# Kernel tuning notes

Measured on AMD Instinct MI355X. Metric: run time of the kernel, lower is better.

The kernel has to match this reference:

```python
import jax, jax.numpy as jnp
import numpy as np

THRESHOLD = 0.1  # init kwarg threshold
N_HITS_PER_EVENT = 200000
N_EVENTS = 64


def setup_inputs() -> dict:
    key = jax.random.key(0)
    n = N_HITS_PER_EVENT * N_EVENTS
    score = jax.random.uniform(key, (n, 1), dtype=jnp.float32)  # noise score in (0,1)
    row_splits = (jnp.arange(N_EVENTS + 1, dtype=jnp.int32) * N_HITS_PER_EVENT)
    return {"score": score, "row_splits": row_splits}


def reference(score, row_splits):
    """Faithful, fully vectorized version of select_threshold_with_backgather.

    Per segment: keep all vertices with score > threshold PLUS all vertices tied
    with the segment minimum score; non-kept vertices backgather to the FIRST
    kept minimum-score vertex of their segment (new/compacted indexing).
    Returns (sel [M,1], newrs [n_seg+1], backgather [N,1]) in the layer's
    call-output order (sel, newrs, allbackgather).
    """
    s = score[:, 0]
    n = s.shape[0]
    n_seg = row_splits.shape[0] - 1

    # segment id of every vertex from the row splits
    segids = jnp.searchsorted(row_splits, jnp.arange(n, dtype=row_splits.dtype), side='right') - 1
    segids = segids.astype(jnp.int32)

    # per-segment minimum score; ties with the min are all kept (== original isminscore)
    segmin = jax.ops.segment_min(s, segids, num_segments=n_seg)
    ismin = s == segmin[segids]
    keep = (s > THRESHOLD) | ismin

    # global compacted position of each kept vertex (n_previous_rs + local keeprange)
    kept_pos = jnp.cumsum(keep.astype(jnp.int32)) - 1

    # representative = first kept min-score vertex per segment (original minidx + n_previous_rs)
    big = jnp.int32(n)
    rep_pos = jax.ops.segment_min(jnp.where(keep & ismin, kept_pos, big), segids, num_segments=n_seg)

    backgather = jnp.where(keep, kept_pos, rep_pos[segids])

    # selection indices (data-dependent size; computed on concrete values, not under jit)
    sel = jnp.nonzero(keep)[0].astype(jnp.int32)

    counts = jax.ops.segment_sum(keep.astype(jnp.int32), segids, num_segments=n_seg)
    newrs = jnp.concatenate([jnp.zeros((1,), jnp.int32), jnp.cumsum(counts).astype(jnp.int32)])

    return sel[:, None], newrs, backgather[:, None].astype(jnp.int32)
```

## Files before the change

kernel.cpp:

```cpp
#include <hip/hip_runtime.h>
#include <stdint.h>

#define BLOCK 256
#define ITEMS 8
#define TILE (BLOCK * ITEMS)
#define WPB (TILE / 64)
#define MAXSEG 64
#define THRESH 0.1f

typedef unsigned long long u64;

__device__ __forceinline__ int find_seg(const int* rs, int n_seg, int i) {
    int lo = 0, hi = n_seg;
    while (hi - lo > 1) {
        int mid = (lo + hi) >> 1;
        if (rs[mid] <= i) lo = mid; else hi = mid;
    }
    return lo;
}

__global__ __launch_bounds__(BLOCK) void k_pass1(const float* __restrict__ score,
        const int* __restrict__ row_splits, int n_seg, int n, int nwords,
        u64* __restrict__ partial_val, int* __restrict__ partial_seg,
        u64* __restrict__ bitmask, int* __restrict__ block_counts) {
    __shared__ int rs[MAXSEG + 1];
    __shared__ u64 wval[8];
    __shared__ int wseg[8];
    __shared__ int wsum[4];
    for (int j = threadIdx.x; j <= n_seg; j += BLOCK) rs[j] = row_splits[j];
    __syncthreads();
    int lane = threadIdx.x & 63, wv = threadIdx.x >> 6;
    int wbase = blockIdx.x * TILE + wv * 512;
    u64 m0 = ~0ull, m1 = ~0ull, myword = 0;
    int sf = -1, sl = -1, cnt = 0;
    if (wbase < n) {
        int wend = min(n, wbase + 512) - 1;
        sf = find_seg(rs, n_seg, wbase);
        sl = find_seg(rs, n_seg, wend);
        int bval = (sl != sf) ? rs[sf + 1] : 0x7FFFFFFF;
        #pragma unroll
        for (int it = 0; it < 8; it++) {
            int i = wbase + it * 64 + lane;
            bool keep = false;
            if (i < n) {
                float v = score[i];
                u64 p = ((u64)__float_as_uint(v) << 32) | (unsigned int)i;
                if (i < bval) m0 = min(m0, p); else m1 = min(m1, p);
                keep = v > THRESH;
            }
            u64 bal = __ballot(keep);
            if (lane == it) myword = bal;
            cnt += __popcll(bal);
        }
        for (int o = 32; o > 0; o >>= 1) {
            m0 = min(m0, (u64)__shfl_down((unsigned long long)m0, o, 64));
            m1 = min(m1, (u64)__shfl_down((unsigned long long)m1, o, 64));
        }
        if (lane < 8) {
            int w = (wbase >> 6) + lane;
            if (w < nwords) bitmask[w] = myword;
        }
    }
    if (lane == 0) {
        wval[2 * wv] = m0;     wseg[2 * wv] = sf;
        wval[2 * wv + 1] = m1; wseg[2 * wv + 1] = (sl != sf) ? sl : -1;
        wsum[wv] = cnt;
    }
    __syncthreads();
    if (threadIdx.x == 0) {
        int base = blockIdx.x * TILE;
        int endi = min(n, base + TILE) - 1;
        int s0 = find_seg(rs, n_seg, base);
        int s1 = find_seg(rs, n_seg, endi);
        u64 o0 = ~0ull, o1 = ~0ull;
        for (int k = 0; k < 8; k++) {
            if (wseg[k] == s0) o0 = min(o0, wval[k]);
            else if (wseg[k] == s1) o1 = min(o1, wval[k]);
        }
        partial_val[2 * blockIdx.x] = o0;
        partial_seg[2 * blockIdx.x] = s0;
        partial_val[2 * blockIdx.x + 1] = o1;
        partial_seg[2 * blockIdx.x + 1] = (s1 != s0) ? s1 : -1;
        block_counts[blockIdx.x] = wsum[0] + wsum[1] + wsum[2] + wsum[3];
    }
}

__global__ __launch_bounds__(BLOCK) void k_segfix(const float* __restrict__ score,
        const int* __restrict__ row_splits, int n_seg, int n,
        const u64* __restrict__ partial_val, const int* __restrict__ partial_seg,
        u64* __restrict__ seg_packed, u64* __restrict__ bitmask,
        int* __restrict__ block_counts) {
    __shared__ u64 wred[4];
    __shared__ int nmatch;
    __shared__ int mlist[64];
    int s = blockIdx.x;
    int lo = row_splits[s], hi = row_splits[s + 1];
    int lane = threadIdx.x & 63, wv = threadIdx.x >> 6;
    if (threadIdx.x == 0) nmatch = 0;
    u64 m = ~0ull;
    int e0 = 0, e1 = -1;
    if (hi > lo) {
        e0 = 2 * (lo / TILE);
        e1 = 2 * ((hi - 1) / TILE) + 1;
        for (int e = e0 + threadIdx.x; e <= e1; e += BLOCK)
            if (partial_seg[e] == s) m = min(m, partial_val[e]);
    }
    for (int o = 32; o > 0; o >>= 1)
        m = min(m, (u64)__shfl_down((unsigned long long)m, o, 64));
    if (lane == 0) wred[wv] = m;
    __syncthreads();
    if (threadIdx.x == 0) {
        u64 r = min(min(wred[0], wred[1]), min(wred[2], wred[3]));
        wred[0] = r;
        seg_packed[s] = r;
    }
    __syncthreads();
    u64 sp = wred[0];
    if (sp == ~0ull) return;
    unsigned int smb = (unsigned int)(sp >> 32);
    if (__uint_as_float(smb) > THRESH) return;
    for (int e = e0 + threadIdx.x; e <= e1; e += BLOCK) {
        if (partial_seg[e] == s && (unsigned int)(partial_val[e] >> 32) == smb) {
            int k = atomicAdd(&nmatch, 1);
            if (k < 64) mlist[k] = e >> 1;
        }
    }
    __syncthreads();
    int nm = min(nmatch, 64);
    for (int k = 0; k < nm; k++) {
        int b = mlist[k];
        int rlo = max(b * TILE, lo);
        int rhi = min(min((b + 1) * TILE, n), hi);
        int c = 0;
        for (int i = rlo + threadIdx.x; i < rhi; i += BLOCK) {
            if (__float_as_uint(score[i]) == smb) {
                atomicOr(&bitmask[i >> 6], 1ull << (i & 63));
                c++;
            }
        }
        for (int o = 32; o > 0; o >>= 1) c += __shfl_down(c, o, 64);
        if (lane == 0 && c) atomicAdd(&block_counts[b], c);
    }
}

__global__ __launch_bounds__(BLOCK) void k_scan(const int* __restrict__ counts,
                                                int* __restrict__ offsets, int nb) {
    __shared__ int wtot[BLOCK / 64];
    int per = (nb + BLOCK - 1) / BLOCK;
    int s = per * threadIdx.x, e = min(nb, s + per);
    int sum = 0;
    for (int i = s; i < e; i++) sum += counts[i];
    int lane = threadIdx.x & 63, wv = threadIdx.x >> 6;
    int incl = sum;
    for (int o = 1; o < 64; o <<= 1) {
        int t = __shfl_up(incl, o, 64);
        if (lane >= o) incl += t;
    }
    if (lane == 63) wtot[wv] = incl;
    __syncthreads();
    int excl = incl - sum;
    for (int k = 0; k < wv; k++) excl += wtot[k];
    for (int i = s; i < e; i++) { offsets[i] = excl; excl += counts[i]; }
}

__global__ __launch_bounds__(BLOCK) void k_query(const int* __restrict__ row_splits,
        int n_seg, int n, int M,
        const u64* __restrict__ seg_packed, const u64* __restrict__ bitmask,
        const int* __restrict__ block_offsets,
        int* __restrict__ rep_pos, int* __restrict__ newrs_out) {
    int lane = threadIdx.x & 63, wv = threadIdx.x >> 6;
    int q = blockIdx.x * (BLOCK / 64) + wv;
    int nq = 2 * n_seg + 1;
    if (q >= nq) return;
    unsigned int uidx;
    if (q <= n_seg) uidx = (unsigned int)row_splits[q];
    else uidx = (unsigned int)(seg_packed[q - (n_seg + 1)] & 0xFFFFFFFFu);
    int result;
    if (uidx >= (unsigned int)n) {
        result = M;
    } else {
        int idx = (int)uidx;
        int b = idx / TILE;
        int wq = idx >> 6;
        int cnt = 0;
        for (int w = b * WPB + lane; w < wq; w += 64) cnt += __popcll(bitmask[w]);
        if (lane == 0 && (idx & 63))
            cnt += __popcll(bitmask[wq] & ((1ull << (idx & 63)) - 1));
        for (int o = 32; o > 0; o >>= 1) cnt += __shfl_down(cnt, o, 64);
        result = block_offsets[b] + cnt;
    }
    if (lane == 0) {
        if (q <= n_seg) newrs_out[q] = result;
        else rep_pos[q - (n_seg + 1)] = result;
    }
}

__global__ __launch_bounds__(BLOCK) void k_output(const int* __restrict__ row_splits,
        int n_seg, int n,
        const int* __restrict__ rep_pos, const u64* __restrict__ bitmask,
        const int* __restrict__ block_offsets,
        int* __restrict__ sel_out, int* __restrict__ back_out) {
    __shared__ int rs[MAXSEG + 1];
    __shared__ int srep[MAXSEG];
    __shared__ u64 swords[WPB];
    __shared__ int wpre[WPB];
    for (int j = threadIdx.x; j <= n_seg; j += BLOCK) rs[j] = row_splits[j];
    for (int j = threadIdx.x; j < n_seg; j += BLOCK) srep[j] = rep_pos[j];
    int base = blockIdx.x * TILE;
    int nw = min(WPB, (n - base + 63) >> 6);
    for (int j = threadIdx.x; j < nw; j += BLOCK) swords[j] = bitmask[(base >> 6) + j];
    __syncthreads();
    if (threadIdx.x == 0) {
        int acc = 0;
        for (int k = 0; k < nw; k++) { wpre[k] = acc; acc += __popcll(swords[k]); }
    }
    __syncthreads();
    int bo = block_offsets[blockIdx.x];
    int lane = threadIdx.x & 63, wv = threadIdx.x >> 6;
    #pragma unroll
    for (int it = 0; it < 8; it++) {
        int widx = wv * 8 + it;
        int i = base + widx * 64 + lane;
        if (i < n) {
            u64 word = swords[widx];
            bool keep = (word >> lane) & 1;
            int val;
            if (keep) {
                int pos = bo + wpre[widx] + __popcll(word & ((1ull << lane) - 1));
                val = pos;
                sel_out[pos] = i;
            } else {
                int seg = find_seg(rs, n_seg, i);
                val = srep[seg];
            }
            back_out[i] = val;
        }
    }
}

extern "C" void kernel_launch(void* const* d_in, const int* in_sizes, int n_in,
                              void* d_out, int out_size, void* d_ws, size_t ws_size,
                              hipStream_t stream) {
    const float* score = (const float*)d_in[0];
    const int* row_splits = (const int*)d_in[1];
    int n = in_sizes[0];
    int n_seg = in_sizes[1] - 1;
    int M = out_size - (n_seg + 1) - n;
    int nb = (n + TILE - 1) / TILE;
    int nwords = (n + 63) / 64;

    u64* seg_packed   = (u64*)d_ws;
    u64* partial_val  = seg_packed + MAXSEG;
    int* partial_seg  = (int*)(partial_val + 2 * nb);
    int* rep_pos      = partial_seg + 2 * nb;
    int* block_counts = rep_pos + 64;
    int* block_offsets= block_counts + nb;
    uintptr_t bm_addr = (uintptr_t)(block_offsets + nb);
    bm_addr = (bm_addr + 7) & ~(uintptr_t)7;
    u64* bitmask      = (u64*)bm_addr;

    int* out = (int*)d_out;
    int* sel_out   = out;
    int* newrs_out = out + M;
    int* back_out  = out + M + (n_seg + 1);

    hipLaunchKernelGGL(k_pass1, dim3(nb), dim3(BLOCK), 0, stream,
                       score, row_splits, n_seg, n, nwords,
                       partial_val, partial_seg, bitmask, block_counts);
    hipLaunchKernelGGL(k_segfix, dim3(n_seg), dim3(BLOCK), 0, stream,
                       score, row_splits, n_seg, n,
                       partial_val, partial_seg, seg_packed, bitmask, block_counts);
    hipLaunchKernelGGL(k_scan, dim3(1), dim3(BLOCK), 0, stream,
                       block_counts, block_offsets, nb);
    int nq = 2 * n_seg + 1;
    int qblocks = (nq + (BLOCK / 64) - 1) / (BLOCK / 64);
    hipLaunchKernelGGL(k_query, dim3(qblocks), dim3(BLOCK), 0, stream,
                       row_splits, n_seg, n, M, seg_packed, bitmask,
                       block_offsets, rep_pos, newrs_out);
    hipLaunchKernelGGL(k_output, dim3(nb), dim3(BLOCK), 0, stream,
                       row_splits, n_seg, n, rep_pos, bitmask,
                       block_offsets, sel_out, back_out);
}
```

Baseline: 186.9 us.

## Fuse scan with query kernel and stage output writes through shared memory

```diff
diff --git a/kernel.cpp b/kernel.cpp
--- a/kernel.cpp
+++ b/kernel.cpp
@@ -143,53 +143,48 @@
     }
 }
 
-__global__ __launch_bounds__(BLOCK) void k_scan(const int* __restrict__ counts,
-                                                int* __restrict__ offsets, int nb) {
+__global__ __launch_bounds__(BLOCK) void k_scanq(const int* __restrict__ counts,
+        int* __restrict__ offsets, int nb,
+        const int* __restrict__ row_splits, int n_seg, int n, int M,
+        const u64* __restrict__ seg_packed, const u64* __restrict__ bitmask,
+        int* __restrict__ rep_pos, int* __restrict__ newrs_out) {
     __shared__ int wtot[BLOCK / 64];
-    int per = (nb + BLOCK - 1) / BLOCK;
-    int s = per * threadIdx.x, e = min(nb, s + per);
-    int sum = 0;
-    for (int i = s; i < e; i++) sum += counts[i];
     int lane = threadIdx.x & 63, wv = threadIdx.x >> 6;
-    int incl = sum;
-    for (int o = 1; o < 64; o <<= 1) {
-        int t = __shfl_up(incl, o, 64);
-        if (lane >= o) incl += t;
-    }
-    if (lane == 63) wtot[wv] = incl;
-    __syncthreads();
-    int excl = incl - sum;
-    for (int k = 0; k < wv; k++) excl += wtot[k];
-    for (int i = s; i < e; i++) { offsets[i] = excl; excl += counts[i]; }
-}
-
-__global__ __launch_bounds__(BLOCK) void k_query(const int* __restrict__ row_splits,
-        int n_seg, int n, int M,
-        const u64* __restrict__ seg_packed, const u64* __restrict__ bitmask,
-        const int* __restrict__ block_offsets,
-        int* __restrict__ rep_pos, int* __restrict__ newrs_out) {
-    int lane = threadIdx.x & 63, wv = threadIdx.x >> 6;
-    int q = blockIdx.x * (BLOCK / 64) + wv;
+    {
+        int per = (nb + BLOCK - 1) / BLOCK;
+        int s = per * threadIdx.x, e = min(nb, s + per);
+        int sum = 0;
+        for (int i = s; i < e; i++) sum += counts[i];
+        int incl = sum;
+        for (int o = 1; o < 64; o <<= 1) {
+            int t = __shfl_up(incl, o, 64);
+            if (lane >= o) incl += t;
+        }
+        if (lane == 63) wtot[wv] = incl;
+        __syncthreads();
+        int excl = incl - sum;
+        for (int k = 0; k < wv; k++) excl += wtot[k];
+        for (int i = s; i < e; i++) { offsets[i] = excl; excl += counts[i]; }
+    }
+    __syncthreads();
     int nq = 2 * n_seg + 1;
-    if (q >= nq) return;
-    unsigned int uidx;
-    if (q <= n_seg) uidx = (unsigned int)row_splits[q];
-    else uidx = (unsigned int)(seg_packed[q - (n_seg + 1)] & 0xFFFFFFFFu);
-    int result;
-    if (uidx >= (unsigned int)n) {
-        result = M;
-    } else {
-        int idx = (int)uidx;
-        int b = idx / TILE;
-        int wq = idx >> 6;
-        int cnt = 0;
-        for (int w = b * WPB + lane; w < wq; w += 64) cnt += __popcll(bitmask[w]);
-        if (lane == 0 && (idx & 63))
-            cnt += __popcll(bitmask[wq] & ((1ull << (idx & 63)) - 1));
-        for (int o = 32; o > 0; o >>= 1) cnt += __shfl_down(cnt, o, 64);
-        result = block_offsets[b] + cnt;
-    }
-    if (lane == 0) {
+    int q = threadIdx.x;
+    if (q < nq) {
+        unsigned int uidx;
+        if (q <= n_seg) uidx = (unsigned int)row_splits[q];
+        else uidx = (unsigned int)(seg_packed[q - (n_seg + 1)] & 0xFFFFFFFFu);
+        int result;
+        if (uidx >= (unsigned int)n) {
+            result = M;
+        } else {
+            int idx = (int)uidx;
+            int b = idx / TILE;
+            int wq = idx >> 6;
+            int cnt = offsets[b];
+            for (int w = b * WPB; w < wq; w++) cnt += __popcll(bitmask[w]);
+            if (idx & 63) cnt += __popcll(bitmask[wq] & ((1ull << (idx & 63)) - 1));
+            result = cnt;
+        }
         if (q <= n_seg) newrs_out[q] = result;
         else rep_pos[q - (n_seg + 1)] = result;
     }
@@ -204,15 +199,20 @@
     __shared__ int srep[MAXSEG];
     __shared__ u64 swords[WPB];
     __shared__ int wpre[WPB];
+    __shared__ int stot;
+    __shared__ int sbg[TILE];
+    __shared__ int skel[TILE];
     for (int j = threadIdx.x; j <= n_seg; j += BLOCK) rs[j] = row_splits[j];
     for (int j = threadIdx.x; j < n_seg; j += BLOCK) srep[j] = rep_pos[j];
     int base = blockIdx.x * TILE;
-    int nw = min(WPB, (n - base + 63) >> 6);
+    int lim = min(TILE, n - base);
+    int nw = (lim + 63) >> 6;
     for (int j = threadIdx.x; j < nw; j += BLOCK) swords[j] = bitmask[(base >> 6) + j];
     __syncthreads();
     if (threadIdx.x == 0) {
         int acc = 0;
         for (int k = 0; k < nw; k++) { wpre[k] = acc; acc += __popcll(swords[k]); }
+        stot = acc;
     }
     __syncthreads();
     int bo = block_offsets[blockIdx.x];
@@ -224,17 +224,41 @@
         if (i < n) {
             u64 word = swords[widx];
             bool keep = (word >> lane) & 1;
-            int val;
             if (keep) {
-                int pos = bo + wpre[widx] + __popcll(word & ((1ull << lane) - 1));
-                val = pos;
-                sel_out[pos] = i;
+                int loc = wpre[widx] + __popcll(word & ((1ull << lane) - 1));
+                sbg[i - base] = bo + loc;
+                skel[loc] = i;
             } else {
                 int seg = find_seg(rs, n_seg, i);
-                val = srep[seg];
+                sbg[i - base] = srep[seg];
             }
-            back_out[i] = val;
-        }
+        }
+    }
+    __syncthreads();
+    {
+        uintptr_t addr = (uintptr_t)(back_out + base);
+        int st = (int)((4 - ((addr >> 2) & 3)) & 3);
+        if (st > lim) st = lim;
+        int nv = (lim - st) >> 2;
+        for (int t = threadIdx.x; t < nv; t += BLOCK) {
+            int j = st + 4 * t;
+            *(int4*)(back_out + base + j) = make_int4(sbg[j], sbg[j+1], sbg[j+2], sbg[j+3]);
+        }
+        for (int j = threadIdx.x; j < st; j += BLOCK) back_out[base + j] = sbg[j];
+        for (int j = st + 4 * nv + threadIdx.x; j < lim; j += BLOCK) back_out[base + j] = sbg[j];
+    }
+    {
+        int tot = stot;
+        uintptr_t addr = (uintptr_t)(sel_out + bo);
+        int st = (int)((4 - ((addr >> 2) & 3)) & 3);
+        if (st > tot) st = tot;
+        int nv = (tot - st) >> 2;
+        for (int t = threadIdx.x; t < nv; t += BLOCK) {
+            int j = st + 4 * t;
+            *(int4*)(sel_out + bo + j) = make_int4(skel[j], skel[j+1], skel[j+2], skel[j+3]);
+        }
+        for (int j = threadIdx.x; j < st; j += BLOCK) sel_out[bo + j] = skel[j];
+        for (int j = st + 4 * nv + threadIdx.x; j < tot; j += BLOCK) sel_out[bo + j] = skel[j];
     }
 }
 
@@ -270,13 +294,10 @@
     hipLaunchKernelGGL(k_segfix, dim3(n_seg), dim3(BLOCK), 0, stream,
                        score, row_splits, n_seg, n,
                        partial_val, partial_seg, seg_packed, bitmask, block_counts);
-    hipLaunchKernelGGL(k_scan, dim3(1), dim3(BLOCK), 0, stream,
-                       block_counts, block_offsets, nb);
-    int nq = 2 * n_seg + 1;
-    int qblocks = (nq + (BLOCK / 64) - 1) / (BLOCK / 64);
-    hipLaunchKernelGGL(k_query, dim3(qblocks), dim3(BLOCK), 0, stream,
+    hipLaunchKernelGGL(k_scanq, dim3(1), dim3(BLOCK), 0, stream,
+                       block_counts, block_offsets, nb,
                        row_splits, n_seg, n, M, seg_packed, bitmask,
-                       block_offsets, rep_pos, newrs_out);
+                       rep_pos, newrs_out);
     hipLaunchKernelGGL(k_output, dim3(nb), dim3(BLOCK), 0, stream,
                        row_splits, n_seg, n, rep_pos, bitmask,
                        block_offsets, sel_out, back_out);
```

Result: slower. 215.3 us (+15.2%).
